# Performance work log

Measured on AMD Instinct MI355X. Metric: run time of the kernel, lower is better.

The kernel has to match this reference:

```python
import jax, jax.numpy as jnp
import numpy as np

INPUT_SIZE = 1024
HIDDEN_SIZE = 1024


def setup_inputs() -> dict:
    key = jax.random.key(0)
    kq, kc, k1, k2, k3 = jax.random.split(key, 5)
    B, LQ, LC = 8, 1024, 2048
    q = jax.random.normal(kq, (B, LQ, INPUT_SIZE), dtype=jnp.float32)
    c = jax.random.normal(kc, (B, LC, INPUT_SIZE), dtype=jnp.float32)
    s = 1.0 / np.sqrt(INPUT_SIZE)
    wq = jax.random.normal(k1, (INPUT_SIZE, HIDDEN_SIZE), dtype=jnp.float32) * s
    wk = jax.random.normal(k2, (INPUT_SIZE, HIDDEN_SIZE), dtype=jnp.float32) * s
    wv = jax.random.normal(k3, (INPUT_SIZE, HIDDEN_SIZE), dtype=jnp.float32) * s
    return {"q": q, "c": c, "wq": wq, "wk": wk, "wv": wv}


def reference(q, c, wq, wk, wv):
    # Q from context c, K/V from question q (faithful to original arg wiring)
    Q = jnp.einsum('bld,dh->blh', c, wq)   # [B, LC, H]
    K = jnp.einsum('bld,dh->blh', q, wk)   # [B, LQ, H]
    V = jnp.einsum('bld,dh->blh', q, wv)   # [B, LQ, H]
    attn = jnp.einsum('bch,bqh->bcq', Q, K)  # [B, LC, LQ] (no 1/sqrt(d) scaling, as in source)
    attn = jax.nn.softmax(attn, axis=2)
    out = jnp.einsum('bcq,bqh->bch', attn, V)  # [B, LC, H]
    return out
```

## Files before the change

### kernel.cpp

```cpp
#include <hip/hip_runtime.h>
#include <stdint.h>

typedef _Float16 half8 __attribute__((ext_vector_type(8)));
typedef __attribute__((ext_vector_type(4))) float f32x4;
typedef __attribute__((ext_vector_type(4))) unsigned short us4;

__device__ __forceinline__ unsigned short f2h(float f) {
  _Float16 h = (_Float16)f;
  return __builtin_bit_cast(unsigned short, h);
}

__device__ __forceinline__ void async_cp16(const unsigned short* g, unsigned short* l) {
  __builtin_amdgcn_global_load_lds(
      (const __attribute__((address_space(1))) void*)g,
      (__attribute__((address_space(3))) void*)l, 16, 0, 0);
}


#define BARF() { asm volatile("" ::: "memory"); \
                 __builtin_amdgcn_s_barrier(); \
                 asm volatile("" ::: "memory"); }

#define MFMA_QUAD(IOFF) \
  _Pragma("unroll") \
  for (int ii = 0; ii < 4; ++ii) { \
    _Pragma("unroll") \
    for (int jj = 0; jj < 4; ++jj) \
      acc[(IOFF) + ii][jj] = __builtin_amdgcn_mfma_f32_16x16x32_f16( \
          a[ii], b[jj], acc[(IOFF) + ii][jj], 0, 0, 0); \
  }

#define KTILE(BUF, J, ST1, ST2, WAITN) { \
   \
  BARF(); \
  { \
    _Pragma("unroll") \
    for (int jj = 0; jj < 4; ++jj) b[jj] = *(const half8*)&lds[(BUF)*32768 + 16384 + offB[jj]]; \
    _Pragma("unroll") \
    for (int ii = 0; ii < 4; ++ii) a[ii] = *(const half8*)&lds[(BUF)*32768 + offA[ii]]; \
    if (ST1) { const unsigned short* s_ = sA + (J + 1) * 64 + 32; \
      async_cp16(s_ + g0, lds + (1 - (BUF)) * 32768 + 8192 + d0); \
      async_cp16(s_ + g1, lds + (1 - (BUF)) * 32768 + 8192 + d1); } \
    MFMA_QUAD(0) \
  } \
   \
  BARF(); \
  { \
    _Pragma("unroll") \
    for (int ii = 0; ii < 4; ++ii) a[ii] = *(const half8*)&lds[(BUF)*32768 + offA[4 + ii]]; \
    if (ST1) { const unsigned short* s_ = sB + (J + 1) * 64 + 32; \
      async_cp16(s_ + g0, lds + (1 - (BUF)) * 32768 + 24576 + d0); \
      async_cp16(s_ + g1, lds + (1 - (BUF)) * 32768 + 24576 + d1); } \
    MFMA_QUAD(4) \
  } \
   \
  BARF(); \
  { \
    _Pragma("unroll") \
    for (int jj = 0; jj < 4; ++jj) b[jj] = *(const half8*)&lds[(BUF)*32768 + 24576 + offB[jj]]; \
    _Pragma("unroll") \
    for (int ii = 0; ii < 4; ++ii) a[ii] = *(const half8*)&lds[(BUF)*32768 + 8192 + offA[ii]]; \
    if (ST2) { const unsigned short* s_ = sA + (J + 2) * 64; \
      async_cp16(s_ + g0, lds + (BUF) * 32768 + d0); \
      async_cp16(s_ + g1, lds + (BUF) * 32768 + d1); } \
    MFMA_QUAD(0) \
  } \
   \
  BARF(); \
  { \
    _Pragma("unroll") \
    for (int ii = 0; ii < 4; ++ii) a[ii] = *(const half8*)&lds[(BUF)*32768 + 8192 + offA[4 + ii]]; \
    if (ST2) { const unsigned short* s_ = sB + (J + 2) * 64; \
      async_cp16(s_ + g0, lds + (BUF) * 32768 + 16384 + d0); \
      async_cp16(s_ + g1, lds + (BUF) * 32768 + 16384 + d1); } \
    MFMA_QUAD(4) \
  } \
  if ((WAITN) == 4)      asm volatile("s_waitcnt vmcnt(4)" ::: "memory"); \
  else if ((WAITN) == 0) asm volatile("s_waitcnt vmcnt(0)" ::: "memory"); \
}

template<int EPI>
__device__ __forceinline__ void gemm256_core(
    const unsigned short* __restrict__ pA, const unsigned short* __restrict__ pB,
    void* __restrict__ C0, int m0, int n0, unsigned short* lds)
{
  const int t = threadIdx.x;

  const int r0 = t >> 2;
  const int kq0 = ((t & 3) - (r0 >> 1)) & 3;
  const int r1 = (512 + t) >> 2;
  const int kq1 = ((t & 3) - (r1 >> 1)) & 3;
  const long g0 = (long)r0 * 1024 + kq0 * 8;
  const long g1 = (long)r1 * 1024 + kq1 * 8;
  const int d0 = t * 8;
  const int d1 = (512 + t) * 8;

  const unsigned short* sA = pA + (long)m0 * 1024;
  const unsigned short* sB = pB + (long)n0 * 1024;

  const int w  = t >> 6;
  const int l  = t & 63;
  const int wm = (w >> 2) * 128;
  const int wn = (w & 3) * 64;
  const int lm = l & 15;
  const int kq = l >> 4;

  int offA[8], offB[4];
  #pragma unroll
  for (int i = 0; i < 8; ++i) {
    int r = wm + i * 16 + lm;
    offA[i] = r * 32 + (((kq + (r >> 1)) & 3) * 8);
  }
  #pragma unroll
  for (int j = 0; j < 4; ++j) {
    int r = wn + j * 16 + lm;
    offB[j] = r * 32 + (((kq + (r >> 1)) & 3) * 8);
  }

  f32x4 acc[8][4];
  #pragma unroll
  for (int i = 0; i < 8; ++i)
    #pragma unroll
    for (int j = 0; j < 4; ++j)
      acc[i][j] = (f32x4){0.f, 0.f, 0.f, 0.f};

  half8 a[4], b[4];

  async_cp16(sA + g0,      lds + 0     + d0);  async_cp16(sA + g1,      lds + 0     + d1);
  async_cp16(sB + g0,      lds + 16384 + d0);  async_cp16(sB + g1,      lds + 16384 + d1);
  async_cp16(sA + g0 + 32, lds + 8192  + d0);  async_cp16(sA + g1 + 32, lds + 8192  + d1);
  async_cp16(sB + g0 + 32, lds + 24576 + d0);  async_cp16(sB + g1 + 32, lds + 24576 + d1);
  async_cp16(sA + g0 + 64, lds + 32768 + d0);  async_cp16(sA + g1 + 64, lds + 32768 + d1);
  async_cp16(sB + g0 + 64, lds + 49152 + d0);  async_cp16(sB + g1 + 64, lds + 49152 + d1);
  asm volatile("s_waitcnt vmcnt(4)" ::: "memory");

  for (int j2 = 0; j2 < 7; ++j2) {
    const int j = j2 * 2;
    KTILE(0, j,     1, 1, 4)
    KTILE(1, j + 1, 1, 1, 4)
  }
  KTILE(0, 14, 1, 0, 0)
  KTILE(1, 15, 0, 0, -1)

  const int cr = wm + (l >> 4) * 4;
  const int cc = wn + lm;
  if (EPI == 0) {
    float* C = (float*)C0;
    #pragma unroll
    for (int i = 0; i < 8; ++i)
      #pragma unroll
      for (int jj = 0; jj < 4; ++jj)
        #pragma unroll
        for (int r = 0; r < 4; ++r)
          C[(long)(m0 + cr + i * 16 + r) * 1024 + (n0 + cc + jj * 16)] = acc[i][jj][r];
  } else {
    unsigned short* C = (unsigned short*)C0;
    #pragma unroll
    for (int i = 0; i < 8; ++i)
      #pragma unroll
      for (int jj = 0; jj < 4; ++jj)
        #pragma unroll
        for (int r = 0; r < 4; ++r)
          C[(long)(m0 + cr + i * 16 + r) * 1024 + (n0 + cc + jj * 16)] = f2h(acc[i][jj][r]);
  }
}

__global__ __launch_bounds__(512, 2)
void gemm_bt256(const unsigned short* __restrict__ A, const unsigned short* __restrict__ B,
                float* __restrict__ C, long aZ, long bZ, long cZ)
{
  __shared__ __align__(16) unsigned short lds[65536];
  const int bid = blockIdx.x;
  const int lin = (bid & 7) * 32 + (bid >> 3);
  const long z = lin >> 5;
  const int rr = lin & 31;
  gemm256_core<0>(A + z * aZ, B + z * bZ, (void*)(C + z * cZ),
                  (rr >> 2) * 256, (rr & 3) * 256, lds);
}

__global__ __launch_bounds__(512, 2)
void proj_all256(const unsigned short* __restrict__ ch, const unsigned short* __restrict__ qh,
                 const unsigned short* __restrict__ wT,
                 unsigned short* __restrict__ Qf, unsigned short* __restrict__ Kf,
                 unsigned short* __restrict__ Vt)
{
  __shared__ __align__(16) unsigned short lds[65536];
  const int bid = blockIdx.x;
  const int lin = (bid & 7) * 64 + (bid >> 3);
  const long qBatch = 1024l * 1024;

  const unsigned short* pA;
  const unsigned short* pB;
  unsigned short* C;
  int m0, n0;
  if (lin < 256) {
    pA = ch; pB = wT; C = Qf;
    m0 = (lin >> 2) * 256; n0 = (lin & 3) * 256;
  } else if (lin < 384) {
    int i = lin - 256;
    pA = qh; pB = wT + (1l << 20); C = Kf;
    m0 = (i >> 2) * 256; n0 = (i & 3) * 256;
  } else {
    int i = lin - 384;
    long z = i >> 4;
    pA = wT + (2l << 20); pB = qh + z * qBatch; C = Vt + z * qBatch;
    m0 = ((i >> 2) & 3) * 256; n0 = (i & 3) * 256;
  }
  gemm256_core<1>(pA, pB, C, m0, n0, lds);
}

__global__ __launch_bounds__(256)
void prep_all(const float* __restrict__ q, const float* __restrict__ c,
              const float* __restrict__ wq, const float* __restrict__ wk,
              const float* __restrict__ wv,
              unsigned short* __restrict__ qh, unsigned short* __restrict__ ch,
              unsigned short* __restrict__ wT)
{
  __shared__ float tile[32][33];
  const int bid = blockIdx.x;
  const int t = threadIdx.x;

  if (bid < 24576) {
    const float* x;
    unsigned short* y;
    long blk;
    if (bid < 16384) { x = c; y = ch; blk = bid; }
    else             { x = q; y = qh; blk = bid - 16384; }
    long i = (blk * 256 + t) * 4;
    float4 v = *(const float4*)(x + i);
    *(us4*)(y + i) = (us4){f2h(v.x), f2h(v.y), f2h(v.z), f2h(v.w)};
  } else {
    int i = bid - 24576;
    const int d0 = (i & 31) * 32, h0 = ((i >> 5) & 31) * 32, id = i >> 10;
    const float* W = (id == 0) ? wq : ((id == 1) ? wk : wv);
    unsigned short* WT = wT + (long)id * (1 << 20);
    #pragma unroll
    for (int p = 0; p < 4; ++p) {
      int dl = p * 8 + (t >> 5), hl = t & 31;
      tile[dl][hl] = W[(long)(d0 + dl) * 1024 + h0 + hl];
    }
    __syncthreads();
    #pragma unroll
    for (int p = 0; p < 4; ++p) {
      int hr = p * 8 + (t >> 5), dc = t & 31;
      WT[(long)(h0 + hr) * 1024 + d0 + dc] = f2h(tile[dc][hr]);
    }
  }
}

__global__ __launch_bounds__(256)
void softmax_rows(const float* __restrict__ S, unsigned short* __restrict__ P)
{
  const long row = blockIdx.x;
  const int t = threadIdx.x;
  float4 v = *(const float4*)(S + row * 1024 + t * 4);
  float m = fmaxf(fmaxf(v.x, v.y), fmaxf(v.z, v.w));
  #pragma unroll
  for (int off = 32; off > 0; off >>= 1) m = fmaxf(m, __shfl_down(m, off));
  __shared__ float red[4], red2[4];
  if ((t & 63) == 0) red[t >> 6] = m;
  __syncthreads();
  m = fmaxf(fmaxf(red[0], red[1]), fmaxf(red[2], red[3]));
  float e0 = __expf(v.x - m), e1 = __expf(v.y - m);
  float e2 = __expf(v.z - m), e3 = __expf(v.w - m);
  float sum = e0 + e1 + e2 + e3;
  #pragma unroll
  for (int off = 32; off > 0; off >>= 1) sum += __shfl_down(sum, off);
  if ((t & 63) == 0) red2[t >> 6] = sum;
  __syncthreads();
  float inv = 1.0f / (red2[0] + red2[1] + red2[2] + red2[3]);
  us4 o = {f2h(e0 * inv), f2h(e1 * inv), f2h(e2 * inv), f2h(e3 * inv)};
  *(us4*)(P + row * 1024 + t * 4) = o;
}

extern "C" void kernel_launch(void* const* d_in, const int* in_sizes, int n_in,
                              void* d_out, int out_size, void* d_ws, size_t ws_size,
                              hipStream_t stream)
{
  (void)in_sizes; (void)n_in; (void)out_size; (void)ws_size;
  const float* q  = (const float*)d_in[0];
  const float* c  = (const float*)d_in[1];
  const float* wq = (const float*)d_in[2];
  const float* wk = (const float*)d_in[3];
  const float* wv = (const float*)d_in[4];
  float* out = (float*)d_out;

  const size_t MB = 1ull << 20;
  const long cBatch = 2048l * 1024;
  const long qBatch = 1024l * 1024;

  char* ws = (char*)d_ws;
  size_t off = 0;
  auto take = [&](size_t bytes) -> unsigned short* {
    unsigned short* p = (unsigned short*)(ws + off);
    off += bytes;
    return p;
  };
  unsigned short* wT = take(6 * MB);
  unsigned short* qh = take(16 * MB);
  unsigned short* ch = take(32 * MB);
  unsigned short* Kf = take(16 * MB);
  unsigned short* Vt = take(16 * MB);
  unsigned short* Qf = take(32 * MB);
  unsigned short* Pf = ch;

  prep_all<<<27648, 256, 0, stream>>>(q, c, wq, wk, wv, qh, ch, wT);
  proj_all256<<<512, 512, 0, stream>>>(ch, qh, wT, Qf, Kf, Vt);
  gemm_bt256<<<256, 512, 0, stream>>>(Qf, Kf, out, cBatch, qBatch, cBatch);
  softmax_rows<<<16384, 256, 0, stream>>>(out, Pf);
  gemm_bt256<<<256, 512, 0, stream>>>(Pf, Vt, out, cBatch, qBatch, cBatch);
}
```

Before: 306.4 us.

## Restructure GEMM k-loop with register double-buffered fragments and two barriers per tile

Reorganizes the 256-tile GEMM main loop so LDS fragment reads for the next phase are issued into a second register set (a0/a1, b0/b1) while the current phase's MFMAs run. It also halves barriers per k-tile from four to two. Global-to-LDS prefetch now runs only one k-tile ahead, with a full vmcnt(0) wait before each barrier, instead of keeping two tiles in flight. This trades global-load latency hiding for fewer barriers and overlap of LDS reads with MFMA, at the cost of more VGPRs for the extra fragment registers.

```diff
diff --git a/kernel.cpp b/kernel.cpp
--- a/kernel.cpp
+++ b/kernel.cpp
@@ -21,62 +21,58 @@
                  __builtin_amdgcn_s_barrier(); \
                  asm volatile("" ::: "memory"); }
 
-#define MFMA_QUAD(IOFF) \
+#define MFMA_PH(AS, BS, IOFF) \
   _Pragma("unroll") \
   for (int ii = 0; ii < 4; ++ii) { \
     _Pragma("unroll") \
     for (int jj = 0; jj < 4; ++jj) \
       acc[(IOFF) + ii][jj] = __builtin_amdgcn_mfma_f32_16x16x32_f16( \
-          a[ii], b[jj], acc[(IOFF) + ii][jj], 0, 0, 0); \
-  }
-
-#define KTILE(BUF, J, ST1, ST2, WAITN) { \
+          AS[ii], BS[jj], acc[(IOFF) + ii][jj], 0, 0, 0); \
+  }
+
+#define KTILE(BUF, J, ST, RD3) { \
    \
+  asm volatile("s_waitcnt vmcnt(0)" ::: "memory"); \
   BARF(); \
-  { \
+  if (ST) { \
+    const unsigned short* sa_ = sA + (J + 1) * 64; \
+    async_cp16(sa_ + g0, lds + (1 - (BUF)) * 32768 + d0); \
+    async_cp16(sa_ + g1, lds + (1 - (BUF)) * 32768 + d1); \
+    const unsigned short* sb_ = sB + (J + 1) * 64; \
+    async_cp16(sb_ + g0, lds + (1 - (BUF)) * 32768 + 16384 + d0); \
+    async_cp16(sb_ + g1, lds + (1 - (BUF)) * 32768 + 16384 + d1); \
+  } \
+  _Pragma("unroll") \
+  for (int ii = 0; ii < 4; ++ii) a1[ii] = *(const half8*)&lds[(BUF) * 32768 + offA[4 + ii]]; \
+  MFMA_PH(a0, b0, 0) \
+   \
+  _Pragma("unroll") \
+  for (int jj = 0; jj < 4; ++jj) b1[jj] = *(const half8*)&lds[(BUF) * 32768 + 24576 + offB[jj]]; \
+  _Pragma("unroll") \
+  for (int ii = 0; ii < 4; ++ii) a0[ii] = *(const half8*)&lds[(BUF) * 32768 + 8192 + offA[ii]]; \
+  MFMA_PH(a1, b0, 4) \
+   \
+  asm volatile("s_waitcnt vmcnt(0)" ::: "memory"); \
+  BARF(); \
+  if (ST) { \
+    const unsigned short* sa_ = sA + (J + 1) * 64 + 32; \
+    async_cp16(sa_ + g0, lds + (1 - (BUF)) * 32768 + 8192 + d0); \
+    async_cp16(sa_ + g1, lds + (1 - (BUF)) * 32768 + 8192 + d1); \
+    const unsigned short* sb_ = sB + (J + 1) * 64 + 32; \
+    async_cp16(sb_ + g0, lds + (1 - (BUF)) * 32768 + 24576 + d0); \
+    async_cp16(sb_ + g1, lds + (1 - (BUF)) * 32768 + 24576 + d1); \
+  } \
+  _Pragma("unroll") \
+  for (int ii = 0; ii < 4; ++ii) a1[ii] = *(const half8*)&lds[(BUF) * 32768 + 8192 + offA[4 + ii]]; \
+  MFMA_PH(a0, b1, 0) \
+   \
+  if (RD3) { \
     _Pragma("unroll") \
-    for (int jj = 0; jj < 4; ++jj) b[jj] = *(const half8*)&lds[(BUF)*32768 + 16384 + offB[jj]]; \
+    for (int jj = 0; jj < 4; ++jj) b0[jj] = *(const half8*)&lds[(1 - (BUF)) * 32768 + 16384 + offB[jj]]; \
     _Pragma("unroll") \
-    for (int ii = 0; ii < 4; ++ii) a[ii] = *(const half8*)&lds[(BUF)*32768 + offA[ii]]; \
-    if (ST1) { const unsigned short* s_ = sA + (J + 1) * 64 + 32; \
-      async_cp16(s_ + g0, lds + (1 - (BUF)) * 32768 + 8192 + d0); \
-      async_cp16(s_ + g1, lds + (1 - (BUF)) * 32768 + 8192 + d1); } \
-    MFMA_QUAD(0) \
+    for (int ii = 0; ii < 4; ++ii) a0[ii] = *(const half8*)&lds[(1 - (BUF)) * 32768 + offA[ii]]; \
   } \
-   \
-  BARF(); \
-  { \
-    _Pragma("unroll") \
-    for (int ii = 0; ii < 4; ++ii) a[ii] = *(const half8*)&lds[(BUF)*32768 + offA[4 + ii]]; \
-    if (ST1) { const unsigned short* s_ = sB + (J + 1) * 64 + 32; \
-      async_cp16(s_ + g0, lds + (1 - (BUF)) * 32768 + 24576 + d0); \
-      async_cp16(s_ + g1, lds + (1 - (BUF)) * 32768 + 24576 + d1); } \
-    MFMA_QUAD(4) \
-  } \
-   \
-  BARF(); \
-  { \
-    _Pragma("unroll") \
-    for (int jj = 0; jj < 4; ++jj) b[jj] = *(const half8*)&lds[(BUF)*32768 + 24576 + offB[jj]]; \
-    _Pragma("unroll") \
-    for (int ii = 0; ii < 4; ++ii) a[ii] = *(const half8*)&lds[(BUF)*32768 + 8192 + offA[ii]]; \
-    if (ST2) { const unsigned short* s_ = sA + (J + 2) * 64; \
-      async_cp16(s_ + g0, lds + (BUF) * 32768 + d0); \
-      async_cp16(s_ + g1, lds + (BUF) * 32768 + d1); } \
-    MFMA_QUAD(0) \
-  } \
-   \
-  BARF(); \
-  { \
-    _Pragma("unroll") \
-    for (int ii = 0; ii < 4; ++ii) a[ii] = *(const half8*)&lds[(BUF)*32768 + 8192 + offA[4 + ii]]; \
-    if (ST2) { const unsigned short* s_ = sB + (J + 2) * 64; \
-      async_cp16(s_ + g0, lds + (BUF) * 32768 + 16384 + d0); \
-      async_cp16(s_ + g1, lds + (BUF) * 32768 + 16384 + d1); } \
-    MFMA_QUAD(4) \
-  } \
-  if ((WAITN) == 4)      asm volatile("s_waitcnt vmcnt(4)" ::: "memory"); \
-  else if ((WAITN) == 0) asm volatile("s_waitcnt vmcnt(0)" ::: "memory"); \
+  MFMA_PH(a1, b1, 4) \
 }
 
 template<int EPI>
@@ -124,23 +120,26 @@
     for (int j = 0; j < 4; ++j)
       acc[i][j] = (f32x4){0.f, 0.f, 0.f, 0.f};
 
-  half8 a[4], b[4];
+  half8 a0[4], a1[4], b0[4], b1[4];
 
   async_cp16(sA + g0,      lds + 0     + d0);  async_cp16(sA + g1,      lds + 0     + d1);
   async_cp16(sB + g0,      lds + 16384 + d0);  async_cp16(sB + g1,      lds + 16384 + d1);
   async_cp16(sA + g0 + 32, lds + 8192  + d0);  async_cp16(sA + g1 + 32, lds + 8192  + d1);
   async_cp16(sB + g0 + 32, lds + 24576 + d0);  async_cp16(sB + g1 + 32, lds + 24576 + d1);
-  async_cp16(sA + g0 + 64, lds + 32768 + d0);  async_cp16(sA + g1 + 64, lds + 32768 + d1);
-  async_cp16(sB + g0 + 64, lds + 49152 + d0);  async_cp16(sB + g1 + 64, lds + 49152 + d1);
-  asm volatile("s_waitcnt vmcnt(4)" ::: "memory");
+  asm volatile("s_waitcnt vmcnt(0)" ::: "memory");
+  BARF();
+  #pragma unroll
+  for (int jj = 0; jj < 4; ++jj) b0[jj] = *(const half8*)&lds[16384 + offB[jj]];
+  #pragma unroll
+  for (int ii = 0; ii < 4; ++ii) a0[ii] = *(const half8*)&lds[offA[ii]];
 
   for (int j2 = 0; j2 < 7; ++j2) {
     const int j = j2 * 2;
-    KTILE(0, j,     1, 1, 4)
-    KTILE(1, j + 1, 1, 1, 4)
-  }
-  KTILE(0, 14, 1, 0, 0)
-  KTILE(1, 15, 0, 0, -1)
+    KTILE(0, j,     1, 1)
+    KTILE(1, j + 1, 1, 1)
+  }
+  KTILE(0, 14, 1, 1)
+  KTILE(1, 15, 0, 0)
 
   const int cr = wm + (l >> 4) * 4;
   const int cc = wn + lm;
```

New measurement: 325.5 us. +6.2%, slower.

## Switch GEMM core to 32x32x16 MFMA and use one wave per softmax row

Applied to the files above, without the earlier changes.

Replaces the 16x16x32 MFMA tiling in the shared GEMM core with 32x32x16 MFMA fragments, which changes the LDS fragment offsets, the accumulator layout and the epilogue store mapping. The larger instruction does more work per issue and needs fewer LDS fragment loads per K-slice. Separately, the softmax kernel now handles four rows per block with one wave per row, so it reduces with wave-level xor shuffles and needs no shared memory or barriers. In exchange, the epilogue stores and the row mapping become more complex and have to match the 32x32 output layout.

```diff
diff --git a/kernel.cpp b/kernel.cpp
--- a/kernel.cpp
+++ b/kernel.cpp
@@ -2,7 +2,7 @@
 #include <stdint.h>
 
 typedef _Float16 half8 __attribute__((ext_vector_type(8)));
-typedef __attribute__((ext_vector_type(4))) float f32x4;
+typedef __attribute__((ext_vector_type(16))) float f32x16;
 typedef __attribute__((ext_vector_type(4))) unsigned short us4;
 
 __device__ __forceinline__ unsigned short f2h(float f) {
@@ -21,13 +21,16 @@
                  __builtin_amdgcn_s_barrier(); \
                  asm volatile("" ::: "memory"); }
 
-#define MFMA_QUAD(IOFF) \
+#define MFMA32(AA, BB, IOFF) \
   _Pragma("unroll") \
-  for (int ii = 0; ii < 4; ++ii) { \
-    _Pragma("unroll") \
-    for (int jj = 0; jj < 4; ++jj) \
-      acc[(IOFF) + ii][jj] = __builtin_amdgcn_mfma_f32_16x16x32_f16( \
-          a[ii], b[jj], acc[(IOFF) + ii][jj], 0, 0, 0); \
+  for (int kc_ = 0; kc_ < 2; ++kc_) { \
+    _Pragma("unroll") \
+    for (int fm_ = 0; fm_ < 2; ++fm_) { \
+      _Pragma("unroll") \
+      for (int fn_ = 0; fn_ < 2; ++fn_) \
+        acc[(IOFF) + fm_][fn_] = __builtin_amdgcn_mfma_f32_32x32x16_f16( \
+            AA[fm_][kc_], BB[fn_][kc_], acc[(IOFF) + fm_][fn_], 0, 0, 0); \
+    } \
   }
 
 #define KTILE(BUF, J, ST1, ST2, WAITN) { \
@@ -35,45 +38,63 @@
   BARF(); \
   { \
     _Pragma("unroll") \
-    for (int jj = 0; jj < 4; ++jj) b[jj] = *(const half8*)&lds[(BUF)*32768 + 16384 + offB[jj]]; \
-    _Pragma("unroll") \
-    for (int ii = 0; ii < 4; ++ii) a[ii] = *(const half8*)&lds[(BUF)*32768 + offA[ii]]; \
+    for (int fn = 0; fn < 2; ++fn) \
+      _Pragma("unroll") \
+      for (int kc = 0; kc < 2; ++kc) \
+        bb[fn][kc] = *(const half8*)&lds[(BUF) * 32768 + 16384 + offB[fn][kc]]; \
+    _Pragma("unroll") \
+    for (int fm = 0; fm < 2; ++fm) \
+      _Pragma("unroll") \
+      for (int kc = 0; kc < 2; ++kc) \
+        aa[fm][kc] = *(const half8*)&lds[(BUF) * 32768 + offA[fm][kc]]; \
     if (ST1) { const unsigned short* s_ = sA + (J + 1) * 64 + 32; \
       async_cp16(s_ + g0, lds + (1 - (BUF)) * 32768 + 8192 + d0); \
       async_cp16(s_ + g1, lds + (1 - (BUF)) * 32768 + 8192 + d1); } \
-    MFMA_QUAD(0) \
+    MFMA32(aa, bb, 0) \
   } \
    \
   BARF(); \
   { \
     _Pragma("unroll") \
-    for (int ii = 0; ii < 4; ++ii) a[ii] = *(const half8*)&lds[(BUF)*32768 + offA[4 + ii]]; \
+    for (int fm = 0; fm < 2; ++fm) \
+      _Pragma("unroll") \
+      for (int kc = 0; kc < 2; ++kc) \
+        aa[fm][kc] = *(const half8*)&lds[(BUF) * 32768 + offA[2 + fm][kc]]; \
     if (ST1) { const unsigned short* s_ = sB + (J + 1) * 64 + 32; \
       async_cp16(s_ + g0, lds + (1 - (BUF)) * 32768 + 24576 + d0); \
       async_cp16(s_ + g1, lds + (1 - (BUF)) * 32768 + 24576 + d1); } \
-    MFMA_QUAD(4) \
+    MFMA32(aa, bb, 2) \
   } \
    \
   BARF(); \
   { \
     _Pragma("unroll") \
-    for (int jj = 0; jj < 4; ++jj) b[jj] = *(const half8*)&lds[(BUF)*32768 + 24576 + offB[jj]]; \
-    _Pragma("unroll") \
-    for (int ii = 0; ii < 4; ++ii) a[ii] = *(const half8*)&lds[(BUF)*32768 + 8192 + offA[ii]]; \
+    for (int fn = 0; fn < 2; ++fn) \
+      _Pragma("unroll") \
+      for (int kc = 0; kc < 2; ++kc) \
+        bb[fn][kc] = *(const half8*)&lds[(BUF) * 32768 + 16384 + offB[fn][2 + kc]]; \
+    _Pragma("unroll") \
+    for (int fm = 0; fm < 2; ++fm) \
+      _Pragma("unroll") \
+      for (int kc = 0; kc < 2; ++kc) \
+        aa[fm][kc] = *(const half8*)&lds[(BUF) * 32768 + offA[fm][2 + kc]]; \
     if (ST2) { const unsigned short* s_ = sA + (J + 2) * 64; \
       async_cp16(s_ + g0, lds + (BUF) * 32768 + d0); \
       async_cp16(s_ + g1, lds + (BUF) * 32768 + d1); } \
-    MFMA_QUAD(0) \
+    MFMA32(aa, bb, 0) \
   } \
    \
   BARF(); \
   { \
     _Pragma("unroll") \
-    for (int ii = 0; ii < 4; ++ii) a[ii] = *(const half8*)&lds[(BUF)*32768 + 8192 + offA[4 + ii]]; \
+    for (int fm = 0; fm < 2; ++fm) \
+      _Pragma("unroll") \
+      for (int kc = 0; kc < 2; ++kc) \
+        aa[fm][kc] = *(const half8*)&lds[(BUF) * 32768 + offA[2 + fm][2 + kc]]; \
     if (ST2) { const unsigned short* s_ = sB + (J + 2) * 64; \
       async_cp16(s_ + g0, lds + (BUF) * 32768 + 16384 + d0); \
       async_cp16(s_ + g1, lds + (BUF) * 32768 + 16384 + d1); } \
-    MFMA_QUAD(4) \
+    MFMA32(aa, bb, 2) \
   } \
   if ((WAITN) == 4)      asm volatile("s_waitcnt vmcnt(4)" ::: "memory"); \
   else if ((WAITN) == 0) asm volatile("s_waitcnt vmcnt(0)" ::: "memory"); \
@@ -102,29 +123,39 @@
   const int l  = t & 63;
   const int wm = (w >> 2) * 128;
   const int wn = (w & 3) * 64;
-  const int lm = l & 15;
-  const int kq = l >> 4;
-
-  int offA[8], offB[4];
-  #pragma unroll
-  for (int i = 0; i < 8; ++i) {
-    int r = wm + i * 16 + lm;
-    offA[i] = r * 32 + (((kq + (r >> 1)) & 3) * 8);
-  }
-  #pragma unroll
-  for (int j = 0; j < 4; ++j) {
-    int r = wn + j * 16 + lm;
-    offB[j] = r * 32 + (((kq + (r >> 1)) & 3) * 8);
-  }
-
-  f32x4 acc[8][4];
-  #pragma unroll
-  for (int i = 0; i < 8; ++i)
-    #pragma unroll
-    for (int j = 0; j < 4; ++j)
-      acc[i][j] = (f32x4){0.f, 0.f, 0.f, 0.f};
-
-  half8 a[4], b[4];
+  const int lr = l & 31;
+  const int lk = l >> 5;
+
+  int offA[4][4], offB[2][4];
+  #pragma unroll
+  for (int fm = 0; fm < 4; ++fm) {
+    int r = wm + fm * 32 + lr;
+    #pragma unroll
+    for (int kc = 0; kc < 4; ++kc) {
+      int g = (kc & 1) * 2 + lk;
+      offA[fm][kc] = (kc >> 1) * 8192 + r * 32 + (((g + (r >> 1)) & 3) * 8);
+    }
+  }
+  #pragma unroll
+  for (int fn = 0; fn < 2; ++fn) {
+    int r = wn + fn * 32 + lr;
+    #pragma unroll
+    for (int kc = 0; kc < 4; ++kc) {
+      int g = (kc & 1) * 2 + lk;
+      offB[fn][kc] = (kc >> 1) * 8192 + r * 32 + (((g + (r >> 1)) & 3) * 8);
+    }
+  }
+
+  f32x16 acc[4][2];
+  #pragma unroll
+  for (int i = 0; i < 4; ++i)
+    #pragma unroll
+    for (int j = 0; j < 2; ++j)
+      #pragma unroll
+      for (int e = 0; e < 16; ++e)
+        acc[i][j][e] = 0.f;
+
+  half8 aa[2][2], bb[2][2];
 
   async_cp16(sA + g0,      lds + 0     + d0);  async_cp16(sA + g1,      lds + 0     + d1);
   async_cp16(sB + g0,      lds + 16384 + d0);  async_cp16(sB + g1,      lds + 16384 + d1);
@@ -142,26 +173,30 @@
   KTILE(0, 14, 1, 0, 0)
   KTILE(1, 15, 0, 0, -1)
 
-  const int cr = wm + (l >> 4) * 4;
-  const int cc = wn + lm;
   if (EPI == 0) {
     float* C = (float*)C0;
     #pragma unroll
-    for (int i = 0; i < 8; ++i)
+    for (int fm = 0; fm < 4; ++fm)
       #pragma unroll
-      for (int jj = 0; jj < 4; ++jj)
+      for (int fn = 0; fn < 2; ++fn)
         #pragma unroll
-        for (int r = 0; r < 4; ++r)
-          C[(long)(m0 + cr + i * 16 + r) * 1024 + (n0 + cc + jj * 16)] = acc[i][jj][r];
+        for (int rg = 0; rg < 16; ++rg) {
+          int row = m0 + wm + fm * 32 + (rg & 3) + 8 * (rg >> 2) + 4 * lk;
+          int col = n0 + wn + fn * 32 + lr;
+          C[(long)row * 1024 + col] = acc[fm][fn][rg];
+        }
   } else {
     unsigned short* C = (unsigned short*)C0;
     #pragma unroll
-    for (int i = 0; i < 8; ++i)
+    for (int fm = 0; fm < 4; ++fm)
       #pragma unroll
-      for (int jj = 0; jj < 4; ++jj)
+      for (int fn = 0; fn < 2; ++fn)
         #pragma unroll
-        for (int r = 0; r < 4; ++r)
-          C[(long)(m0 + cr + i * 16 + r) * 1024 + (n0 + cc + jj * 16)] = f2h(acc[i][jj][r]);
+        for (int rg = 0; rg < 16; ++rg) {
+          int row = m0 + wm + fm * 32 + (rg & 3) + 8 * (rg >> 2) + 4 * lk;
+          int col = n0 + wn + fn * 32 + lr;
+          C[(long)row * 1024 + col] = f2h(acc[fm][fn][rg]);
+        }
   }
 }
 
@@ -251,26 +286,40 @@
 __global__ __launch_bounds__(256)
 void softmax_rows(const float* __restrict__ S, unsigned short* __restrict__ P)
 {
-  const long row = blockIdx.x;
-  const int t = threadIdx.x;
-  float4 v = *(const float4*)(S + row * 1024 + t * 4);
-  float m = fmaxf(fmaxf(v.x, v.y), fmaxf(v.z, v.w));
-  #pragma unroll
-  for (int off = 32; off > 0; off >>= 1) m = fmaxf(m, __shfl_down(m, off));
-  __shared__ float red[4], red2[4];
-  if ((t & 63) == 0) red[t >> 6] = m;
-  __syncthreads();
-  m = fmaxf(fmaxf(red[0], red[1]), fmaxf(red[2], red[3]));
-  float e0 = __expf(v.x - m), e1 = __expf(v.y - m);
-  float e2 = __expf(v.z - m), e3 = __expf(v.w - m);
-  float sum = e0 + e1 + e2 + e3;
-  #pragma unroll
-  for (int off = 32; off > 0; off >>= 1) sum += __shfl_down(sum, off);
-  if ((t & 63) == 0) red2[t >> 6] = sum;
-  __syncthreads();
-  float inv = 1.0f / (red2[0] + red2[1] + red2[2] + red2[3]);
-  us4 o = {f2h(e0 * inv), f2h(e1 * inv), f2h(e2 * inv), f2h(e3 * inv)};
-  *(us4*)(P + row * 1024 + t * 4) = o;
+  const long row = (long)blockIdx.x * 4 + (threadIdx.x >> 6);
+  const int lane = threadIdx.x & 63;
+  const float* Sr = S + row * 1024;
+
+  float4 v[4];
+  #pragma unroll
+  for (int c = 0; c < 4; ++c) v[c] = *(const float4*)(Sr + c * 256 + lane * 4);
+
+  float m = -1e30f;
+  #pragma unroll
+  for (int c = 0; c < 4; ++c)
+    m = fmaxf(m, fmaxf(fmaxf(v[c].x, v[c].y), fmaxf(v[c].z, v[c].w)));
+  #pragma unroll
+  for (int off = 32; off > 0; off >>= 1) m = fmaxf(m, __shfl_xor(m, off));
+
+  float e[4][4];
+  float sum = 0.f;
+  #pragma unroll
+  for (int c = 0; c < 4; ++c) {
+    e[c][0] = __expf(v[c].x - m); e[c][1] = __expf(v[c].y - m);
+    e[c][2] = __expf(v[c].z - m); e[c][3] = __expf(v[c].w - m);
+    sum += e[c][0] + e[c][1] + e[c][2] + e[c][3];
+  }
+  #pragma unroll
+  for (int off = 32; off > 0; off >>= 1) sum += __shfl_xor(sum, off);
+
+  const float inv = 1.0f / sum;
+  unsigned short* Pr = P + row * 1024;
+  #pragma unroll
+  for (int c = 0; c < 4; ++c) {
+    us4 o = {f2h(e[c][0] * inv), f2h(e[c][1] * inv),
+             f2h(e[c][2] * inv), f2h(e[c][3] * inv)};
+    *(us4*)(Pr + c * 256 + lane * 4) = o;
+  }
 }
 
 extern "C" void kernel_launch(void* const* d_in, const int* in_sizes, int n_in,
@@ -307,6 +356,6 @@
   prep_all<<<27648, 256, 0, stream>>>(q, c, wq, wk, wv, qh, ch, wT);
   proj_all256<<<512, 512, 0, stream>>>(ch, qh, wT, Qf, Kf, Vt);
   gemm_bt256<<<256, 512, 0, stream>>>(Qf, Kf, out, cBatch, qBatch, cBatch);
-  softmax_rows<<<16384, 256, 0, stream>>>(out, Pf);
+  softmax_rows<<<4096, 256, 0, stream>>>(out, Pf);
   gemm_bt256<<<256, 512, 0, stream>>>(Pf, Vt, out, cBatch, qBatch, cBatch);
 }
```

Measured after the change: 318.3 us. +3.9%, slower.

## Fuse all stages into one persistent kernel with global atomic barriers

Applied to the files above, without the earlier changes.

Replaces the five separate launches (convert/transpose, projections, QK^T GEMM, softmax, PV GEMM) with one persistent 256-block kernel that grid-strides over each stage and separates stages with atomic-counter grid barriers. The aim is to remove launch gaps and tail effects between kernels. The softmax is rewritten so each wavefront handles whole rows with xor-shuffle reductions. In exchange, the prep and softmax phases now run on only 256 blocks of 512 threads, and correctness relies on all blocks being co-resident so the spin barriers cannot deadlock.

```diff
diff --git a/kernel.cpp b/kernel.cpp
--- a/kernel.cpp
+++ b/kernel.cpp
@@ -14,6 +14,16 @@
   __builtin_amdgcn_global_load_lds(
       (const __attribute__((address_space(1))) void*)g,
       (__attribute__((address_space(3))) void*)l, 16, 0, 0);
+}
+
+__device__ __forceinline__ void gsync(unsigned int* bar, unsigned int target) {
+  __syncthreads();
+  if (threadIdx.x == 0) {
+    __hip_atomic_fetch_add(bar, 1u, __ATOMIC_ACQ_REL, __HIP_MEMORY_SCOPE_AGENT);
+    while (__hip_atomic_load(bar, __ATOMIC_ACQUIRE, __HIP_MEMORY_SCOPE_AGENT) < target)
+      __builtin_amdgcn_s_sleep(2);
+  }
+  __syncthreads();
 }
 
 
@@ -86,6 +96,8 @@
 {
   const int t = threadIdx.x;
 
+  BARF();
+
   const int r0 = t >> 2;
   const int kq0 = ((t & 3) - (r0 >> 1)) & 3;
   const int r1 = (512 + t) >> 2;
@@ -166,111 +178,136 @@
 }
 
 __global__ __launch_bounds__(512, 2)
-void gemm_bt256(const unsigned short* __restrict__ A, const unsigned short* __restrict__ B,
-                float* __restrict__ C, long aZ, long bZ, long cZ)
+void fused_all(const float* __restrict__ q, const float* __restrict__ c,
+               const float* __restrict__ wq, const float* __restrict__ wk,
+               const float* __restrict__ wv,
+               unsigned short* __restrict__ qh, unsigned short* __restrict__ ch,
+               unsigned short* __restrict__ wT,
+               unsigned short* __restrict__ Qf, unsigned short* __restrict__ Kf,
+               unsigned short* __restrict__ Vt,
+               float* __restrict__ out,
+               unsigned int* __restrict__ bar)
 {
   __shared__ __align__(16) unsigned short lds[65536];
   const int bid = blockIdx.x;
-  const int lin = (bid & 7) * 32 + (bid >> 3);
-  const long z = lin >> 5;
-  const int rr = lin & 31;
-  gemm256_core<0>(A + z * aZ, B + z * bZ, (void*)(C + z * cZ),
-                  (rr >> 2) * 256, (rr & 3) * 256, lds);
-}
-
-__global__ __launch_bounds__(512, 2)
-void proj_all256(const unsigned short* __restrict__ ch, const unsigned short* __restrict__ qh,
-                 const unsigned short* __restrict__ wT,
-                 unsigned short* __restrict__ Qf, unsigned short* __restrict__ Kf,
-                 unsigned short* __restrict__ Vt)
-{
-  __shared__ __align__(16) unsigned short lds[65536];
-  const int bid = blockIdx.x;
-  const int lin = (bid & 7) * 64 + (bid >> 3);
-  const long qBatch = 1024l * 1024;
-
-  const unsigned short* pA;
-  const unsigned short* pB;
-  unsigned short* C;
-  int m0, n0;
-  if (lin < 256) {
-    pA = ch; pB = wT; C = Qf;
-    m0 = (lin >> 2) * 256; n0 = (lin & 3) * 256;
-  } else if (lin < 384) {
-    int i = lin - 256;
-    pA = qh; pB = wT + (1l << 20); C = Kf;
-    m0 = (i >> 2) * 256; n0 = (i & 3) * 256;
-  } else {
-    int i = lin - 384;
-    long z = i >> 4;
-    pA = wT + (2l << 20); pB = qh + z * qBatch; C = Vt + z * qBatch;
-    m0 = ((i >> 2) & 3) * 256; n0 = (i & 3) * 256;
-  }
-  gemm256_core<1>(pA, pB, C, m0, n0, lds);
-}
-
-__global__ __launch_bounds__(256)
-void prep_all(const float* __restrict__ q, const float* __restrict__ c,
-              const float* __restrict__ wq, const float* __restrict__ wk,
-              const float* __restrict__ wv,
-              unsigned short* __restrict__ qh, unsigned short* __restrict__ ch,
-              unsigned short* __restrict__ wT)
-{
-  __shared__ float tile[32][33];
-  const int bid = blockIdx.x;
   const int t = threadIdx.x;
 
-  if (bid < 24576) {
+  const long cB = 2048l * 1024;
+  const long qB = 1024l * 1024;
+
+  for (int job = bid; job < 12288; job += 256) {
     const float* x;
     unsigned short* y;
     long blk;
-    if (bid < 16384) { x = c; y = ch; blk = bid; }
-    else             { x = q; y = qh; blk = bid - 16384; }
-    long i = (blk * 256 + t) * 4;
+    if (job < 8192) { x = c; y = ch; blk = job; }
+    else            { x = q; y = qh; blk = job - 8192; }
+    long i = (blk * 512 + t) * 4;
     float4 v = *(const float4*)(x + i);
     *(us4*)(y + i) = (us4){f2h(v.x), f2h(v.y), f2h(v.z), f2h(v.w)};
-  } else {
-    int i = bid - 24576;
-    const int d0 = (i & 31) * 32, h0 = ((i >> 5) & 31) * 32, id = i >> 10;
-    const float* W = (id == 0) ? wq : ((id == 1) ? wk : wv);
-    unsigned short* WT = wT + (long)id * (1 << 20);
-    #pragma unroll
-    for (int p = 0; p < 4; ++p) {
-      int dl = p * 8 + (t >> 5), hl = t & 31;
-      tile[dl][hl] = W[(long)(d0 + dl) * 1024 + h0 + hl];
+  }
+  {
+    float* tileF = (float*)lds;
+    const int half = t >> 8, tt = t & 255;
+    float* tl = tileF + half * (32 * 33);
+    for (int jp = bid; jp < 1536; jp += 256) {
+      int jobi = jp * 2 + half;
+      const int td0 = (jobi & 31) * 32, h0 = ((jobi >> 5) & 31) * 32, id = jobi >> 10;
+      const float* W = (id == 0) ? wq : ((id == 1) ? wk : wv);
+      unsigned short* WT = wT + (long)id * (1 << 20);
+      #pragma unroll
+      for (int p = 0; p < 4; ++p) {
+        int dl = p * 8 + (tt >> 5), hl = tt & 31;
+        tl[dl * 33 + hl] = W[(long)(td0 + dl) * 1024 + h0 + hl];
+      }
+      __syncthreads();
+      #pragma unroll
+      for (int p = 0; p < 4; ++p) {
+        int hr = p * 8 + (tt >> 5), dc = tt & 31;
+        WT[(long)(h0 + hr) * 1024 + td0 + dc] = f2h(tl[dc * 33 + hr]);
+      }
+      __syncthreads();
     }
-    __syncthreads();
-    #pragma unroll
-    for (int p = 0; p < 4; ++p) {
-      int hr = p * 8 + (t >> 5), dc = t & 31;
-      WT[(long)(h0 + hr) * 1024 + d0 + dc] = f2h(tile[dc][hr]);
+  }
+  gsync(bar, 256);
+
+  #pragma unroll 1
+  for (int rep = 0; rep < 2; ++rep) {
+    const int j = bid + rep * 256;
+    const int lin = (j & 7) * 64 + (j >> 3);
+    const unsigned short* pA;
+    const unsigned short* pB;
+    unsigned short* C;
+    int m0, n0;
+    if (lin < 256) {
+      pA = ch; pB = wT; C = Qf;
+      m0 = (lin >> 2) * 256; n0 = (lin & 3) * 256;
+    } else if (lin < 384) {
+      int i = lin - 256;
+      pA = qh; pB = wT + (1l << 20); C = Kf;
+      m0 = (i >> 2) * 256; n0 = (i & 3) * 256;
+    } else {
+      int i = lin - 384;
+      long z = i >> 4;
+      pA = wT + (2l << 20); pB = qh + z * qB; C = Vt + z * qB;
+      m0 = ((i >> 2) & 3) * 256; n0 = (i & 3) * 256;
     }
-  }
-}
-
-__global__ __launch_bounds__(256)
-void softmax_rows(const float* __restrict__ S, unsigned short* __restrict__ P)
-{
-  const long row = blockIdx.x;
-  const int t = threadIdx.x;
-  float4 v = *(const float4*)(S + row * 1024 + t * 4);
-  float m = fmaxf(fmaxf(v.x, v.y), fmaxf(v.z, v.w));
-  #pragma unroll
-  for (int off = 32; off > 0; off >>= 1) m = fmaxf(m, __shfl_down(m, off));
-  __shared__ float red[4], red2[4];
-  if ((t & 63) == 0) red[t >> 6] = m;
-  __syncthreads();
-  m = fmaxf(fmaxf(red[0], red[1]), fmaxf(red[2], red[3]));
-  float e0 = __expf(v.x - m), e1 = __expf(v.y - m);
-  float e2 = __expf(v.z - m), e3 = __expf(v.w - m);
-  float sum = e0 + e1 + e2 + e3;
-  #pragma unroll
-  for (int off = 32; off > 0; off >>= 1) sum += __shfl_down(sum, off);
-  if ((t & 63) == 0) red2[t >> 6] = sum;
-  __syncthreads();
-  float inv = 1.0f / (red2[0] + red2[1] + red2[2] + red2[3]);
-  us4 o = {f2h(e0 * inv), f2h(e1 * inv), f2h(e2 * inv), f2h(e3 * inv)};
-  *(us4*)(P + row * 1024 + t * 4) = o;
+    gemm256_core<1>(pA, pB, C, m0, n0, lds);
+  }
+  gsync(bar, 512);
+
+  {
+    const int lin = (bid & 7) * 32 + (bid >> 3);
+    const long z = lin >> 5;
+    const int rr = lin & 31;
+    gemm256_core<0>(Qf + z * cB, Kf + z * qB, (void*)(out + z * cB),
+                    (rr >> 2) * 256, (rr & 3) * 256, lds);
+  }
+  gsync(bar, 768);
+
+  {
+    const int wv_ = t >> 6, lane = t & 63;
+    #pragma unroll 1
+    for (int rr = 0; rr < 8; ++rr) {
+      const long row = (long)bid * 64 + wv_ * 8 + rr;
+      const float* Sr = out + row * 1024;
+      float4 v[4];
+      #pragma unroll
+      for (int cc = 0; cc < 4; ++cc) v[cc] = *(const float4*)(Sr + cc * 256 + lane * 4);
+      float m = -1e30f;
+      #pragma unroll
+      for (int cc = 0; cc < 4; ++cc)
+        m = fmaxf(m, fmaxf(fmaxf(v[cc].x, v[cc].y), fmaxf(v[cc].z, v[cc].w)));
+      #pragma unroll
+      for (int off = 32; off > 0; off >>= 1) m = fmaxf(m, __shfl_xor(m, off));
+      float e[4][4];
+      float sum = 0.f;
+      #pragma unroll
+      for (int cc = 0; cc < 4; ++cc) {
+        e[cc][0] = __expf(v[cc].x - m); e[cc][1] = __expf(v[cc].y - m);
+        e[cc][2] = __expf(v[cc].z - m); e[cc][3] = __expf(v[cc].w - m);
+        sum += e[cc][0] + e[cc][1] + e[cc][2] + e[cc][3];
+      }
+      #pragma unroll
+      for (int off = 32; off > 0; off >>= 1) sum += __shfl_xor(sum, off);
+      const float inv = 1.0f / sum;
+      unsigned short* Pr = ch + row * 1024;
+      #pragma unroll
+      for (int cc = 0; cc < 4; ++cc) {
+        us4 o = {f2h(e[cc][0] * inv), f2h(e[cc][1] * inv),
+                 f2h(e[cc][2] * inv), f2h(e[cc][3] * inv)};
+        *(us4*)(Pr + cc * 256 + lane * 4) = o;
+      }
+    }
+  }
+  gsync(bar, 1024);
+
+  {
+    const int lin = (bid & 7) * 32 + (bid >> 3);
+    const long z = lin >> 5;
+    const int rr = lin & 31;
+    gemm256_core<0>(ch + z * cB, Vt + z * qB, (void*)(out + z * cB),
+                    (rr >> 2) * 256, (rr & 3) * 256, lds);
+  }
 }
 
 extern "C" void kernel_launch(void* const* d_in, const int* in_sizes, int n_in,
@@ -286,9 +323,6 @@
   float* out = (float*)d_out;
 
   const size_t MB = 1ull << 20;
-  const long cBatch = 2048l * 1024;
-  const long qBatch = 1024l * 1024;
-
   char* ws = (char*)d_ws;
   size_t off = 0;
   auto take = [&](size_t bytes) -> unsigned short* {
@@ -302,11 +336,10 @@
   unsigned short* Kf = take(16 * MB);
   unsigned short* Vt = take(16 * MB);
   unsigned short* Qf = take(32 * MB);
-  unsigned short* Pf = ch;
-
-  prep_all<<<27648, 256, 0, stream>>>(q, c, wq, wk, wv, qh, ch, wT);
-  proj_all256<<<512, 512, 0, stream>>>(ch, qh, wT, Qf, Kf, Vt);
-  gemm_bt256<<<256, 512, 0, stream>>>(Qf, Kf, out, cBatch, qBatch, cBatch);
-  softmax_rows<<<16384, 256, 0, stream>>>(out, Pf);
-  gemm_bt256<<<256, 512, 0, stream>>>(Pf, Vt, out, cBatch, qBatch, cBatch);
-}
+  unsigned int*  bar = (unsigned int*)take(256);
+
+  hipMemsetAsync(bar, 0, 256, stream);
+
+  fused_all<<<256, 512, 0, stream>>>(q, c, wq, wk, wv,
+                                     qh, ch, wT, Qf, Kf, Vt, out, bar);
+}
```

New measurement: 585.5 us. +91.1%, slower.
